# Performance work log

Hardware: AMD Instinct MI355X
Metric: run time of the kernel (lower is better)

## Reference

```python
import jax, jax.numpy as jnp
import numpy as np

B, S, IN_F, OUT_F, GROUP = 2, 1024, 4096, 4096, 128
N_GROUPS = IN_F // GROUP  # 32


def setup_inputs() -> dict:
    key = jax.random.key(0)
    k1, k2, k3, k4 = jax.random.split(key, 4)
    x = jax.random.normal(k1, (B, S, IN_F), dtype=jnp.float32)
    # int4-range weights stored in int8, symmetric quant in [-7, 7]
    w_q = jax.random.randint(k2, (OUT_F, N_GROUPS, GROUP), -7, 8, dtype=jnp.int8)
    # per-(group, out_feature) scales, positive
    s_w = jax.random.uniform(k3, (N_GROUPS, OUT_F), dtype=jnp.float32,
                             minval=1e-3, maxval=2e-2)
    bias = jax.random.normal(k4, (OUT_F,), dtype=jnp.float32)
    return {"x": x, "w_q": w_q, "s_w": s_w, "bias": bias}


def reference(x, w_q, s_w, bias):
    # Faithful to QuantLinearW4Grouped.forward:
    #   y_g = einsum('ngk,ogk->ngo', x_f, w_f); y = (y_g * s_w[None]).sum(1) + bias
    # Expressed as a single fused einsum (identical math, no (n,g,o) intermediate).
    prefix = x.shape[:-1]
    orig_dtype = x.dtype
    xg = x.reshape(-1, N_GROUPS, GROUP).astype(jnp.float32)  # (n, g, k)
    w_f = w_q.astype(jnp.float32)                            # (o, g, k)
    y = jnp.einsum('ngk,ogk,go->no', xg, w_f, s_w)           # (n, o)
    y = y + bias.astype(y.dtype)
    return y.reshape(*prefix, OUT_F).astype(orig_dtype)
```

## Files before the change

### kernel.cpp

```cpp
#include <hip/hip_runtime.h>
#include <hip/hip_bf16.h>
#include <stdint.h>

#define M_TOK 2048
#define N_OUT 4096
#define K_IN  4096
#define GROUPSZ 128
#define NGRP  32

typedef signed char i8;
typedef int    intx4  __attribute__((ext_vector_type(4)));
typedef float  floatx4 __attribute__((ext_vector_type(4)));

#define AS1 __attribute__((address_space(1)))
#define AS3 __attribute__((address_space(3)))

#define XQ_BLOCKS (M_TOK)
#define WQ_BLOCKS (N_OUT * K_IN / 16 / 256)

__global__ __launch_bounds__(256) void quant_kernel(
    const float* __restrict__ x, const int* __restrict__ wq,
    i8* __restrict__ xq, i8* __restrict__ wq8, float* __restrict__ sx) {
  __shared__ float red[4];
  int b = blockIdx.x;
  int tid = threadIdx.x;
  if (b < XQ_BLOCKS) {
    const float* xr = x + (size_t)b * K_IN;
    int e0 = tid * 16;
    float4 v0 = *(const float4*)(xr + e0);
    float4 v1 = *(const float4*)(xr + e0 + 4);
    float4 v2 = *(const float4*)(xr + e0 + 8);
    float4 v3 = *(const float4*)(xr + e0 + 12);
    float m = fabsf(v0.x);
    m = fmaxf(m, fabsf(v0.y)); m = fmaxf(m, fabsf(v0.z)); m = fmaxf(m, fabsf(v0.w));
    m = fmaxf(m, fabsf(v1.x)); m = fmaxf(m, fabsf(v1.y)); m = fmaxf(m, fabsf(v1.z)); m = fmaxf(m, fabsf(v1.w));
    m = fmaxf(m, fabsf(v2.x)); m = fmaxf(m, fabsf(v2.y)); m = fmaxf(m, fabsf(v2.z)); m = fmaxf(m, fabsf(v2.w));
    m = fmaxf(m, fabsf(v3.x)); m = fmaxf(m, fabsf(v3.y)); m = fmaxf(m, fabsf(v3.z)); m = fmaxf(m, fabsf(v3.w));
#pragma unroll
    for (int off = 32; off > 0; off >>= 1)
      m = fmaxf(m, __shfl_xor(m, off, 64));
    int lane = tid & 63, wv = tid >> 6;
    if (lane == 0) red[wv] = m;
    __syncthreads();
    m = fmaxf(fmaxf(red[0], red[1]), fmaxf(red[2], red[3]));
    float inv = (m > 0.f) ? 127.f / m : 0.f;
    union { i8 q[16]; int4 v; } u;
    u.q[0]  = (i8)(int)rintf(v0.x * inv); u.q[1]  = (i8)(int)rintf(v0.y * inv);
    u.q[2]  = (i8)(int)rintf(v0.z * inv); u.q[3]  = (i8)(int)rintf(v0.w * inv);
    u.q[4]  = (i8)(int)rintf(v1.x * inv); u.q[5]  = (i8)(int)rintf(v1.y * inv);
    u.q[6]  = (i8)(int)rintf(v1.z * inv); u.q[7]  = (i8)(int)rintf(v1.w * inv);
    u.q[8]  = (i8)(int)rintf(v2.x * inv); u.q[9]  = (i8)(int)rintf(v2.y * inv);
    u.q[10] = (i8)(int)rintf(v2.z * inv); u.q[11] = (i8)(int)rintf(v2.w * inv);
    u.q[12] = (i8)(int)rintf(v3.x * inv); u.q[13] = (i8)(int)rintf(v3.y * inv);
    u.q[14] = (i8)(int)rintf(v3.z * inv); u.q[15] = (i8)(int)rintf(v3.w * inv);
    *(int4*)(xq + (size_t)b * K_IN + e0) = u.v;
    if (tid == 0) sx[b] = m * (1.f / 127.f);
  } else {
    size_t t = (size_t)(b - XQ_BLOCKS) * 256 + tid;
    size_t base = t * 16;
    const int* src = wq + base;
    int4 a0 = *(const int4*)(src);
    int4 a1 = *(const int4*)(src + 4);
    int4 a2 = *(const int4*)(src + 8);
    int4 a3 = *(const int4*)(src + 12);
    union { i8 q[16]; int4 v; } u;
    u.q[0]  = (i8)a0.x; u.q[1]  = (i8)a0.y; u.q[2]  = (i8)a0.z; u.q[3]  = (i8)a0.w;
    u.q[4]  = (i8)a1.x; u.q[5]  = (i8)a1.y; u.q[6]  = (i8)a1.z; u.q[7]  = (i8)a1.w;
    u.q[8]  = (i8)a2.x; u.q[9]  = (i8)a2.y; u.q[10] = (i8)a2.z; u.q[11] = (i8)a2.w;
    u.q[12] = (i8)a3.x; u.q[13] = (i8)a3.y; u.q[14] = (i8)a3.z; u.q[15] = (i8)a3.w;
    *(int4*)(wq8 + base) = u.v;
  }
}

#define BM 128
#define BN 128
#define BK 128
#define NT (K_IN / BK)

__global__ __launch_bounds__(256, 2) void gemm_i8_kernel(
    const i8* __restrict__ Aq, const i8* __restrict__ Bq,
    const float* __restrict__ sx, const float* __restrict__ sw,
    const float* __restrict__ bias, float* __restrict__ C) {
  __shared__ i8 As[2 * BM * BK];
  __shared__ i8 Bs[2 * BN * BK];

  const int tid  = threadIdx.x;
  const int lane = tid & 63;
  const int wave = tid >> 6;
  const int quad = lane >> 4;
  const int l16  = lane & 15;
  const int bm = blockIdx.y;
  const int bn = blockIdx.x;
  const int wm = wave >> 1;
  const int wn = wave & 1;

  const int rowA0 = bm * BM;
  const int rowB0 = bn * BN;

  const i8* srcA[4]; const i8* srcB[4];
#pragma unroll
  for (int i = 0; i < 4; ++i) {
    int chunk = i * 256 + tid;
    int row = chunk >> 3;
    int csw = (chunk & 7) ^ (row & 7);
    srcA[i] = Aq + (size_t)(rowA0 + row) * K_IN + (csw << 4);
    srcB[i] = Bq + (size_t)(rowB0 + row) * K_IN + (csw << 4);
  }
  i8* dstA[4]; i8* dstB[4];
#pragma unroll
  for (int i = 0; i < 4; ++i) {
    dstA[i] = As + (size_t)(i * 256 + wave * 64) * 16;
    dstB[i] = Bs + (size_t)(i * 256 + wave * 64) * 16;
  }

  auto stage = [&](int buf, int t) {
    const size_t ko = (size_t)t * BK;
#pragma unroll
    for (int i = 0; i < 4; ++i)
      __builtin_amdgcn_global_load_lds(
          (const AS1 void*)(srcA[i] + ko),
          (AS3 void*)(dstA[i] + (size_t)buf * (BM * BK)), 16, 0, 0);
#pragma unroll
    for (int i = 0; i < 4; ++i)
      __builtin_amdgcn_global_load_lds(
          (const AS1 void*)(srcB[i] + ko),
          (AS3 void*)(dstB[i] + (size_t)buf * (BN * BK)), 16, 0, 0);
  };

  const float* swp = sw + rowB0 + wn * 64 + l16;

  stage(0, 0);
  float swv_cur[4], swv_nxt[4];
#pragma unroll
  for (int j = 0; j < 4; ++j) swv_cur[j] = swp[j * 16];
  __syncthreads();

  floatx4 master[4][4];
#pragma unroll
  for (int i = 0; i < 4; ++i)
#pragma unroll
    for (int j = 0; j < 4; ++j) master[i][j] = (floatx4)0.0f;

  const intx4 MAGICV = {0x4B400000, 0x4B400000, 0x4B400000, 0x4B400000};
  const float MAGICF = 12582912.0f;

  const int h  = l16 & 7;
  const int x0 = (quad ^ h) << 4;
  const int x1 = x0 ^ 64;

  for (int t = 0; t < NT; ++t) {
    const int cur = t & 1;
    if (t + 1 < NT) {
      stage(cur ^ 1, t + 1);
#pragma unroll
      for (int j = 0; j < 4; ++j)
        swv_nxt[j] = swp[(size_t)(t + 1) * N_OUT + j * 16];
      asm volatile("s_waitcnt vmcnt(12)" ::: "memory");
    } else {
      asm volatile("s_waitcnt vmcnt(0)" ::: "memory");
    }
    __builtin_amdgcn_s_barrier();

    const i8* Ab = As + (size_t)cur * (BM * BK);
    const i8* Bb = Bs + (size_t)cur * (BN * BK);
    intx4 a[4][2], b[4][2];
#pragma unroll
    for (int i = 0; i < 4; ++i) {
      const i8* pa = Ab + (size_t)(wm * 64 + i * 16 + l16) * BK;
      a[i][0] = *(const intx4*)(pa + x0);
      a[i][1] = *(const intx4*)(pa + x1);
    }
#pragma unroll
    for (int j = 0; j < 4; ++j) {
      const i8* pb = Bb + (size_t)(wn * 64 + j * 16 + l16) * BK;
      b[j][0] = *(const intx4*)(pb + x0);
      b[j][1] = *(const intx4*)(pb + x1);
    }

#pragma unroll
    for (int i = 0; i < 4; ++i)
#pragma unroll
      for (int j = 0; j < 4; ++j) {
        intx4 acc = __builtin_amdgcn_mfma_i32_16x16x64_i8(a[i][0], b[j][0], MAGICV, 0, 0, 0);
        acc = __builtin_amdgcn_mfma_i32_16x16x64_i8(a[i][1], b[j][1], acc, 0, 0, 0);
        master[i][j] += (__builtin_bit_cast(floatx4, acc) - MAGICF) * swv_cur[j];
      }
#pragma unroll
    for (int j = 0; j < 4; ++j) swv_cur[j] = swv_nxt[j];

    asm volatile("s_waitcnt lgkmcnt(0)" ::: "memory");
    __builtin_amdgcn_s_barrier();
  }

#pragma unroll
  for (int i = 0; i < 4; ++i) {
    float4 sxv = *(const float4*)(sx + rowA0 + wm * 64 + i * 16 + quad * 4);
#pragma unroll
    for (int j = 0; j < 4; ++j) {
      int col = rowB0 + wn * 64 + j * 16 + l16;
      float bv = bias[col];
      int rloc = wm * 64 + i * 16 + quad * 4;
      C[(size_t)(rowA0 + rloc + 0) * N_OUT + col] = master[i][j][0] * sxv.x + bv;
      C[(size_t)(rowA0 + rloc + 1) * N_OUT + col] = master[i][j][1] * sxv.y + bv;
      C[(size_t)(rowA0 + rloc + 2) * N_OUT + col] = master[i][j][2] * sxv.z + bv;
      C[(size_t)(rowA0 + rloc + 3) * N_OUT + col] = master[i][j][3] * sxv.w + bv;
    }
  }
}

extern "C" void kernel_launch(void* const* d_in, const int* in_sizes, int n_in,
                              void* d_out, int out_size, void* d_ws, size_t ws_size,
                              hipStream_t stream) {
  const float* x    = (const float*)d_in[0];
  const int*   wq   = (const int*)d_in[1];
  const float* sw   = (const float*)d_in[2];
  const float* bias = (const float*)d_in[3];
  float* out = (float*)d_out;

  i8*    xq  = (i8*)d_ws;
  i8*    wq8 = (i8*)((char*)d_ws + (size_t)M_TOK * K_IN);
  float* sx  = (float*)((char*)d_ws + (size_t)M_TOK * K_IN
                                     + (size_t)N_OUT * K_IN);

  {
    int nblocks = XQ_BLOCKS + WQ_BLOCKS;
    quant_kernel<<<nblocks, 256, 0, stream>>>(x, wq, xq, wq8, sx);
  }
  {
    dim3 grid(N_OUT / BN, M_TOK / BM);
    gemm_i8_kernel<<<grid, 256, 0, stream>>>(xq, wq8, sx, sw, bias, out);
  }
}
```

Baseline: 179.4 us.

## Drop LDS double-buffering to single buffer and raise occupancy to four blocks

Replaces the double-buffered LDS pipeline with a single 32KB buffer. Each K-step now syncs, issues the global-to-LDS loads, loads the scales, syncs again, then computes. The launch-bounds minimum rises from two to four blocks per CU, so occupancy rather than in-block prefetch is meant to hide memory latency. In exchange, the load-compute overlap inside a block is lost, each iteration adds a barrier, and tighter register limits may cause spills.

```diff
diff --git a/kernel.cpp b/kernel.cpp
--- a/kernel.cpp
+++ b/kernel.cpp
@@ -77,12 +77,12 @@
 #define BK 128
 #define NT (K_IN / BK)
 
-__global__ __launch_bounds__(256, 2) void gemm_i8_kernel(
+__global__ __launch_bounds__(256, 4) void gemm_i8_kernel(
     const i8* __restrict__ Aq, const i8* __restrict__ Bq,
     const float* __restrict__ sx, const float* __restrict__ sw,
     const float* __restrict__ bias, float* __restrict__ C) {
-  __shared__ i8 As[2 * BM * BK];
-  __shared__ i8 Bs[2 * BN * BK];
+  __shared__ i8 As[BM * BK];
+  __shared__ i8 Bs[BN * BK];
 
   const int tid  = threadIdx.x;
   const int lane = tid & 63;
@@ -113,27 +113,7 @@
     dstB[i] = Bs + (size_t)(i * 256 + wave * 64) * 16;
   }
 
-  auto stage = [&](int buf, int t) {
-    const size_t ko = (size_t)t * BK;
-#pragma unroll
-    for (int i = 0; i < 4; ++i)
-      __builtin_amdgcn_global_load_lds(
-          (const AS1 void*)(srcA[i] + ko),
-          (AS3 void*)(dstA[i] + (size_t)buf * (BM * BK)), 16, 0, 0);
-#pragma unroll
-    for (int i = 0; i < 4; ++i)
-      __builtin_amdgcn_global_load_lds(
-          (const AS1 void*)(srcB[i] + ko),
-          (AS3 void*)(dstB[i] + (size_t)buf * (BN * BK)), 16, 0, 0);
-  };
-
   const float* swp = sw + rowB0 + wn * 64 + l16;
-
-  stage(0, 0);
-  float swv_cur[4], swv_nxt[4];
-#pragma unroll
-  for (int j = 0; j < 4; ++j) swv_cur[j] = swp[j * 16];
-  __syncthreads();
 
   floatx4 master[4][4];
 #pragma unroll
@@ -149,30 +129,34 @@
   const int x1 = x0 ^ 64;
 
   for (int t = 0; t < NT; ++t) {
-    const int cur = t & 1;
-    if (t + 1 < NT) {
-      stage(cur ^ 1, t + 1);
-#pragma unroll
-      for (int j = 0; j < 4; ++j)
-        swv_nxt[j] = swp[(size_t)(t + 1) * N_OUT + j * 16];
-      asm volatile("s_waitcnt vmcnt(12)" ::: "memory");
-    } else {
-      asm volatile("s_waitcnt vmcnt(0)" ::: "memory");
-    }
-    __builtin_amdgcn_s_barrier();
-
-    const i8* Ab = As + (size_t)cur * (BM * BK);
-    const i8* Bb = Bs + (size_t)cur * (BN * BK);
+    __syncthreads();
+    {
+      const size_t ko = (size_t)t * BK;
+#pragma unroll
+      for (int i = 0; i < 4; ++i)
+        __builtin_amdgcn_global_load_lds(
+            (const AS1 void*)(srcA[i] + ko), (AS3 void*)dstA[i], 16, 0, 0);
+#pragma unroll
+      for (int i = 0; i < 4; ++i)
+        __builtin_amdgcn_global_load_lds(
+            (const AS1 void*)(srcB[i] + ko), (AS3 void*)dstB[i], 16, 0, 0);
+    }
+    float swv[4];
+#pragma unroll
+    for (int j = 0; j < 4; ++j)
+      swv[j] = swp[(size_t)t * N_OUT + j * 16];
+    __syncthreads();
+
     intx4 a[4][2], b[4][2];
 #pragma unroll
     for (int i = 0; i < 4; ++i) {
-      const i8* pa = Ab + (size_t)(wm * 64 + i * 16 + l16) * BK;
+      const i8* pa = As + (size_t)(wm * 64 + i * 16 + l16) * BK;
       a[i][0] = *(const intx4*)(pa + x0);
       a[i][1] = *(const intx4*)(pa + x1);
     }
 #pragma unroll
     for (int j = 0; j < 4; ++j) {
-      const i8* pb = Bb + (size_t)(wn * 64 + j * 16 + l16) * BK;
+      const i8* pb = Bs + (size_t)(wn * 64 + j * 16 + l16) * BK;
       b[j][0] = *(const intx4*)(pb + x0);
       b[j][1] = *(const intx4*)(pb + x1);
     }
@@ -183,13 +167,8 @@
       for (int j = 0; j < 4; ++j) {
         intx4 acc = __builtin_amdgcn_mfma_i32_16x16x64_i8(a[i][0], b[j][0], MAGICV, 0, 0, 0);
         acc = __builtin_amdgcn_mfma_i32_16x16x64_i8(a[i][1], b[j][1], acc, 0, 0, 0);
-        master[i][j] += (__builtin_bit_cast(floatx4, acc) - MAGICF) * swv_cur[j];
+        master[i][j] += (__builtin_bit_cast(floatx4, acc) - MAGICF) * swv[j];
       }
-#pragma unroll
-    for (int j = 0; j < 4; ++j) swv_cur[j] = swv_nxt[j];
-
-    asm volatile("s_waitcnt lgkmcnt(0)" ::: "memory");
-    __builtin_amdgcn_s_barrier();
   }
 
 #pragma unroll
```

Measured after the change: 304.8 us. 1.7x slower.

## Split K across wave pairs in int8 GEMM with LDS reduction

Applied to the files above, without the earlier changes.

Doubles the GEMM block to 512 threads (8 waves). Each pair of waves shares a 64x64 output tile and splits the 128-wide K slice into two 64-wide halves, so each wave issues one MFMA per output subtile per iteration instead of two. Partial accumulators are combined through LDS after the main loop, and each wave of the pair then writes half the rows. The intent is more waves per CU to hide latency, at the cost of a duplicate accumulator set per tile, an extra reduction stage with barriers, and duplicated scale multiplies.

```diff
diff --git a/kernel.cpp b/kernel.cpp
--- a/kernel.cpp
+++ b/kernel.cpp
@@ -76,55 +76,54 @@
 #define BN 128
 #define BK 128
 #define NT (K_IN / BK)
-
-__global__ __launch_bounds__(256, 2) void gemm_i8_kernel(
+#define BUFSZ (BM * BK)
+
+__global__ __launch_bounds__(512, 2) void gemm_i8_kernel(
     const i8* __restrict__ Aq, const i8* __restrict__ Bq,
     const float* __restrict__ sx, const float* __restrict__ sw,
     const float* __restrict__ bias, float* __restrict__ C) {
-  __shared__ i8 As[2 * BM * BK];
-  __shared__ i8 Bs[2 * BN * BK];
-
+  __shared__ i8 As[2 * BUFSZ];
+  __shared__ i8 Bs[2 * BUFSZ];
   const int tid  = threadIdx.x;
   const int lane = tid & 63;
   const int wave = tid >> 6;
   const int quad = lane >> 4;
   const int l16  = lane & 15;
+  const int ot   = wave >> 1;
+  const int kgrp = wave & 1;
+  const int wm   = ot >> 1;
+  const int wn   = ot & 1;
   const int bm = blockIdx.y;
   const int bn = blockIdx.x;
-  const int wm = wave >> 1;
-  const int wn = wave & 1;
 
   const int rowA0 = bm * BM;
   const int rowB0 = bn * BN;
 
-  const i8* srcA[4]; const i8* srcB[4];
-#pragma unroll
-  for (int i = 0; i < 4; ++i) {
-    int chunk = i * 256 + tid;
+  const i8* srcA[2]; const i8* srcB[2];
+  i8* dstA[2]; i8* dstB[2];
+#pragma unroll
+  for (int i = 0; i < 2; ++i) {
+    int chunk = i * 512 + tid;
     int row = chunk >> 3;
     int csw = (chunk & 7) ^ (row & 7);
     srcA[i] = Aq + (size_t)(rowA0 + row) * K_IN + (csw << 4);
     srcB[i] = Bq + (size_t)(rowB0 + row) * K_IN + (csw << 4);
-  }
-  i8* dstA[4]; i8* dstB[4];
-#pragma unroll
-  for (int i = 0; i < 4; ++i) {
-    dstA[i] = As + (size_t)(i * 256 + wave * 64) * 16;
-    dstB[i] = Bs + (size_t)(i * 256 + wave * 64) * 16;
+    dstA[i] = As + (size_t)(i * 512 + wave * 64) * 16;
+    dstB[i] = Bs + (size_t)(i * 512 + wave * 64) * 16;
   }
 
   auto stage = [&](int buf, int t) {
     const size_t ko = (size_t)t * BK;
 #pragma unroll
-    for (int i = 0; i < 4; ++i)
+    for (int i = 0; i < 2; ++i)
       __builtin_amdgcn_global_load_lds(
           (const AS1 void*)(srcA[i] + ko),
-          (AS3 void*)(dstA[i] + (size_t)buf * (BM * BK)), 16, 0, 0);
-#pragma unroll
-    for (int i = 0; i < 4; ++i)
+          (AS3 void*)(dstA[i] + (size_t)buf * BUFSZ), 16, 0, 0);
+#pragma unroll
+    for (int i = 0; i < 2; ++i)
       __builtin_amdgcn_global_load_lds(
           (const AS1 void*)(srcB[i] + ko),
-          (AS3 void*)(dstB[i] + (size_t)buf * (BN * BK)), 16, 0, 0);
+          (AS3 void*)(dstB[i] + (size_t)buf * BUFSZ), 16, 0, 0);
   };
 
   const float* swp = sw + rowB0 + wn * 64 + l16;
@@ -144,9 +143,7 @@
   const intx4 MAGICV = {0x4B400000, 0x4B400000, 0x4B400000, 0x4B400000};
   const float MAGICF = 12582912.0f;
 
-  const int h  = l16 & 7;
-  const int x0 = (quad ^ h) << 4;
-  const int x1 = x0 ^ 64;
+  const int xk = (((quad ^ (l16 & 7)) ^ (kgrp << 2)) << 4);
 
   for (int t = 0; t < NT; ++t) {
     const int cur = t & 1;
@@ -155,34 +152,27 @@
 #pragma unroll
       for (int j = 0; j < 4; ++j)
         swv_nxt[j] = swp[(size_t)(t + 1) * N_OUT + j * 16];
-      asm volatile("s_waitcnt vmcnt(12)" ::: "memory");
+      asm volatile("s_waitcnt vmcnt(8)" ::: "memory");
     } else {
       asm volatile("s_waitcnt vmcnt(0)" ::: "memory");
     }
     __builtin_amdgcn_s_barrier();
 
-    const i8* Ab = As + (size_t)cur * (BM * BK);
-    const i8* Bb = Bs + (size_t)cur * (BN * BK);
-    intx4 a[4][2], b[4][2];
-#pragma unroll
-    for (int i = 0; i < 4; ++i) {
-      const i8* pa = Ab + (size_t)(wm * 64 + i * 16 + l16) * BK;
-      a[i][0] = *(const intx4*)(pa + x0);
-      a[i][1] = *(const intx4*)(pa + x1);
-    }
-#pragma unroll
-    for (int j = 0; j < 4; ++j) {
-      const i8* pb = Bb + (size_t)(wn * 64 + j * 16 + l16) * BK;
-      b[j][0] = *(const intx4*)(pb + x0);
-      b[j][1] = *(const intx4*)(pb + x1);
-    }
-
+    const i8* Ab = As + (size_t)cur * BUFSZ;
+    const i8* Bb = Bs + (size_t)cur * BUFSZ;
+    intx4 a[4], b[4];
 #pragma unroll
     for (int i = 0; i < 4; ++i)
-#pragma unroll
-      for (int j = 0; j < 4; ++j) {
-        intx4 acc = __builtin_amdgcn_mfma_i32_16x16x64_i8(a[i][0], b[j][0], MAGICV, 0, 0, 0);
-        acc = __builtin_amdgcn_mfma_i32_16x16x64_i8(a[i][1], b[j][1], acc, 0, 0, 0);
+      a[i] = *(const intx4*)(Ab + (size_t)(wm * 64 + i * 16 + l16) * BK + xk);
+#pragma unroll
+    for (int j = 0; j < 4; ++j)
+      b[j] = *(const intx4*)(Bb + (size_t)(wn * 64 + j * 16 + l16) * BK + xk);
+
+#pragma unroll
+    for (int i = 0; i < 4; ++i)
+#pragma unroll
+      for (int j = 0; j < 4; ++j) {
+        intx4 acc = __builtin_amdgcn_mfma_i32_16x16x64_i8(a[i], b[j], MAGICV, 0, 0, 0);
         master[i][j] += (__builtin_bit_cast(floatx4, acc) - MAGICF) * swv_cur[j];
       }
 #pragma unroll
@@ -192,8 +182,52 @@
     __builtin_amdgcn_s_barrier();
   }
 
-#pragma unroll
-  for (int i = 0; i < 4; ++i) {
+  floatx4* xb = (floatx4*)Bs;
+  const int xbase = (ot * 64 + lane) * 8;
+  if (kgrp == 1) {
+#pragma unroll
+    for (int ii = 0; ii < 2; ++ii)
+#pragma unroll
+      for (int j = 0; j < 4; ++j) {
+        int c = ii * 4 + j;
+        xb[xbase + (c ^ (lane & 7))] = master[ii][j];
+      }
+  }
+  __syncthreads();
+  if (kgrp == 0) {
+#pragma unroll
+    for (int ii = 0; ii < 2; ++ii)
+#pragma unroll
+      for (int j = 0; j < 4; ++j) {
+        int c = ii * 4 + j;
+        master[ii][j] += xb[xbase + (c ^ (lane & 7))];
+      }
+  }
+  __syncthreads();
+  if (kgrp == 0) {
+#pragma unroll
+    for (int ii = 2; ii < 4; ++ii)
+#pragma unroll
+      for (int j = 0; j < 4; ++j) {
+        int c = (ii - 2) * 4 + j;
+        xb[xbase + (c ^ (lane & 7))] = master[ii][j];
+      }
+  }
+  __syncthreads();
+  if (kgrp == 1) {
+#pragma unroll
+    for (int ii = 2; ii < 4; ++ii)
+#pragma unroll
+      for (int j = 0; j < 4; ++j) {
+        int c = (ii - 2) * 4 + j;
+        master[ii][j] += xb[xbase + (c ^ (lane & 7))];
+      }
+  }
+
+  const int i0 = kgrp * 2;
+#pragma unroll
+  for (int ii = 0; ii < 2; ++ii) {
+    int i = i0 + ii;
     float4 sxv = *(const float4*)(sx + rowA0 + wm * 64 + i * 16 + quad * 4);
 #pragma unroll
     for (int j = 0; j < 4; ++j) {
@@ -228,6 +262,6 @@
   }
   {
     dim3 grid(N_OUT / BN, M_TOK / BM);
-    gemm_i8_kernel<<<grid, 256, 0, stream>>>(xq, wq8, sx, sw, bias, out);
+    gemm_i8_kernel<<<grid, 512, 0, stream>>>(xq, wq8, sx, sw, bias, out);
   }
 }
```

New measurement: 239.7 us. 1.34x slower.
